# Kernel optimization log

Hardware: AMD Instinct MI355X
Metric: run time of the kernel (lower is better)

The kernel has to match this reference:

```python
import jax, jax.numpy as jnp
import numpy as np

B, G, T = 4096, 100, 24


def _greedy_dispatch(demand, caps, prices, slack_price):
    """Exact LP solution of: min prices@alloc + slack_price*slack
    s.t. 0<=alloc<=caps, sum(alloc)+slack = demand (per b,t).
    demand: [B,T] (nonneg), caps: [B,G,T], prices: [G], slack_price: scalar.
    Returns alloc [B,G,T], slack [B,T].
    """
    prices_all = jnp.concatenate([prices, slack_price[None]])        # [G+1]
    # slack capacity = demand itself (slack alone can absorb everything)
    caps_all = jnp.concatenate([caps, demand[:, None, :]], axis=1)    # [B,G+1,T]
    order = jnp.argsort(prices_all)                                   # merit order
    caps_s = caps_all[:, order, :]
    before = jnp.cumsum(caps_s, axis=1) - caps_s                      # capacity ahead in merit order
    alloc_s = jnp.clip(demand[:, None, :] - before, 0.0, caps_s)
    inv = jnp.argsort(order)
    alloc = alloc_s[:, inv, :]
    return alloc[:, :-1, :], alloc[:, -1, :]


def setup_inputs() -> dict:
    key = jax.random.key(0)
    k1, k2, k3, k4 = jax.random.split(key, 4)
    R_up = jax.random.uniform(k1, (B, G, T), dtype=jnp.float32)
    R_dn = jax.random.uniform(k2, (B, G, T), dtype=jnp.float32)
    omega_true = jax.random.normal(k3, (B, T), dtype=jnp.float32) * 5.0
    b_G = 10.0 + 40.0 * jax.random.uniform(k4, (G,), dtype=jnp.float32)  # marginal costs $/MWh
    return {
        "R_up": R_up,
        "R_dn": R_dn,
        "omega_true": omega_true,
        "b_G": b_G,
        "voll": jnp.float32(1000.0),
        "vosp": jnp.float32(500.0),
        "rt_up_ratio": jnp.float32(1.5),
        "rt_dn_ratio": jnp.float32(1.2),
    }


def reference(R_up, R_dn, omega_true, b_G, voll, vosp, rt_up_ratio, rt_dn_ratio):
    c_up = rt_up_ratio * b_G                                          # [G]
    c_dn = rt_dn_ratio * b_G                                          # [G]
    dem_up = jnp.maximum(omega_true, 0.0)                             # [B,T]
    dem_dn = jnp.maximum(-omega_true, 0.0)
    du, LS = _greedy_dispatch(dem_up, R_up, c_up, voll)
    dd, SP = _greedy_dispatch(dem_dn, R_dn, c_dn, vosp)
    rt_obj = (jnp.einsum('g,bgt->b', c_up, du)
              + jnp.einsum('g,bgt->b', c_dn, dd)
              + voll * LS.sum(axis=1) + vosp * SP.sum(axis=1))        # [B]
    return du, dd, LS, SP, rt_obj
```

## Files before the change

### kernel.cpp

```cpp
#include <hip/hip_runtime.h>

#define G_ 100
#define T_ 24
#define GP1 101
#define TILE (G_ * T_)
#define VPB (TILE / 4)
#define WPB 4
#define BLOCK (64 * WPB)

typedef float vfloat4 __attribute__((ext_vector_type(4)));

template<int N>
__device__ __forceinline__ void scan_chunk(int k0,
    const float* __restrict__ capp,
    int ord_lo, int ord_hi, float pr_lo, float pr_hi,
    float* __restrict__ ldscol,
    float dem, float& before, float& objp)
{
    int gg[N]; float pr[N], cap[N];
#pragma unroll
    for (int j = 0; j < N; ++j) {
        const int idx = k0 + j;
        if (idx < 64) {
            gg[j] = __builtin_amdgcn_readlane(ord_lo, idx);
            pr[j] = __int_as_float(__builtin_amdgcn_readlane(__float_as_int(pr_lo), idx));
        } else {
            gg[j] = __builtin_amdgcn_readlane(ord_hi, idx - 64);
            pr[j] = __int_as_float(__builtin_amdgcn_readlane(__float_as_int(pr_hi), idx - 64));
        }
    }
#pragma unroll
    for (int j = 0; j < N; ++j) cap[j] = capp[gg[j] * T_];
#pragma unroll
    for (int j = 0; j < N; ++j) {
        float a = fminf(fmaxf(dem - before, 0.f), cap[j]);
        before += cap[j];
        objp = fmaf(pr[j], a, objp);
        ldscol[gg[j] * T_] = a;
    }
}

__global__ __launch_bounds__(BLOCK, 4) void dispatch_kernel(
    const float* __restrict__ R_up, const float* __restrict__ R_dn,
    const float* __restrict__ omega,
    const float* __restrict__ b_G, const float* __restrict__ voll,
    const float* __restrict__ vosp, const float* __restrict__ ru,
    const float* __restrict__ rd,
    float* __restrict__ out, int B)
{
    __shared__ float s_tile[WPB * TILE];
    __shared__ float s_obj[WPB];

    const int tid  = threadIdx.x;

    if (tid < GP1) {
        float mu, md;
        if (tid < G_) { float bg = b_G[tid]; mu = ru[0] * bg; md = rd[0] * bg; }
        else          { mu = voll[0];        md = vosp[0]; }
        s_tile[tid] = mu; s_tile[128 + tid] = md;
    }
    __syncthreads();
    if (tid < GP1) {
        const float mu = s_tile[tid], md = s_tile[128 + tid];
        int r0 = 0, r1 = 0;
        for (int j = 0; j < GP1; ++j) {
            float vu = s_tile[j], vd = s_tile[128 + j];
            r0 += (vu < mu) || (vu == mu && j < tid);
            r1 += (vd < md) || (vd == md && j < tid);
        }
        ((int*)s_tile)[256 + r0] = tid;  s_tile[512 + r0] = mu;
        ((int*)s_tile)[384 + r1] = tid;  s_tile[640 + r1] = md;
    }
    __syncthreads();

    const int w    = tid >> 6;
    const int lane = tid & 63;
    const int b = __builtin_amdgcn_readfirstlane(blockIdx.x * 2 + (w >> 1));
    const int p = __builtin_amdgcn_readfirstlane(w & 1);
    const size_t bgt = (size_t)B * TILE;
    float* __restrict__ tw = &s_tile[w * TILE];

    const int hi_ok = (lane < GP1 - 64);
    const int   ord_lo = ((const int*)s_tile)[256 + p * 128 + lane];
    const int   ord_hi = hi_ok ? ((const int*)s_tile)[256 + p * 128 + 64 + lane] : 0;
    const float pr_lo  = s_tile[512 + p * 128 + lane];
    const float pr_hi  = hi_ok ? s_tile[512 + p * 128 + 64 + lane] : 0.f;
    __syncthreads();

#pragma unroll
    for (int j = 0; j < 9; ++j) *(vfloat4*)&tw[(lane + j * 64) * 4] = (vfloat4)(0.f);
    if (lane < VPB - 576)       *(vfloat4*)&tw[(lane + 576) * 4]    = (vfloat4)(0.f);

    const int t = (lane < T_) ? lane : 0;

    float objp = 0.f;
    if (lane < T_) {
        const float om  = omega[(size_t)b * T_ + t];
        const float dem = p ? fmaxf(-om, 0.f) : fmaxf(om, 0.f);
        const float* __restrict__ capp = (p ? R_dn : R_up) + (size_t)b * TILE + t;
        float* __restrict__ ldscol = tw + t;

        float before = 0.f;
        scan_chunk<16>( 0, capp, ord_lo, ord_hi, pr_lo, pr_hi, ldscol, dem, before, objp);
        bool run = __any(before < dem);
        if (run) { scan_chunk<16>(16, capp, ord_lo, ord_hi, pr_lo, pr_hi, ldscol, dem, before, objp);
                   run = __any(before < dem); }
        if (run) { scan_chunk< 8>(32, capp, ord_lo, ord_hi, pr_lo, pr_hi, ldscol, dem, before, objp);
                   run = __any(before < dem); }
        if (run) { scan_chunk< 8>(40, capp, ord_lo, ord_hi, pr_lo, pr_hi, ldscol, dem, before, objp);
                   run = __any(before < dem); }
        if (run) { scan_chunk< 8>(48, capp, ord_lo, ord_hi, pr_lo, pr_hi, ldscol, dem, before, objp);
                   run = __any(before < dem); }
        if (run) { scan_chunk< 8>(56, capp, ord_lo, ord_hi, pr_lo, pr_hi, ldscol, dem, before, objp);
                   run = __any(before < dem); }
        if (run) { scan_chunk< 8>(64, capp, ord_lo, ord_hi, pr_lo, pr_hi, ldscol, dem, before, objp);
                   run = __any(before < dem); }
        if (run) { scan_chunk< 8>(72, capp, ord_lo, ord_hi, pr_lo, pr_hi, ldscol, dem, before, objp);
                   run = __any(before < dem); }
        if (run) { scan_chunk< 8>(80, capp, ord_lo, ord_hi, pr_lo, pr_hi, ldscol, dem, before, objp);
                   run = __any(before < dem); }
        if (run) { scan_chunk< 8>(88, capp, ord_lo, ord_hi, pr_lo, pr_hi, ldscol, dem, before, objp);
                   run = __any(before < dem); }
        if (run)   scan_chunk< 4>(96, capp, ord_lo, ord_hi, pr_lo, pr_hi, ldscol, dem, before, objp);

        const float slack_pr =
            __int_as_float(__builtin_amdgcn_readlane(__float_as_int(pr_hi), GP1 - 1 - 64));
        float slackv = fmaxf(dem - before, 0.f);
        objp = fmaf(slack_pr, slackv, objp);
        out[2 * bgt + (size_t)p * B * T_ + (size_t)b * T_ + t] = slackv;
    }

#pragma unroll
    for (int off = 32; off; off >>= 1) objp += __shfl_xor(objp, off, 64);
    if (lane == 0) s_obj[w] = objp;

    __builtin_amdgcn_wave_barrier();
    {
        vfloat4* __restrict__ dst = (vfloat4*)out + ((size_t)p * B + b) * VPB;
#pragma unroll
        for (int j = 0; j < 9; ++j)
            dst[lane + j * 64] = *(const vfloat4*)&tw[(lane + j * 64) * 4];
        if (lane < VPB - 576)
            dst[lane + 576] = *(const vfloat4*)&tw[(lane + 576) * 4];
    }

    __syncthreads();
    if (tid == 0)
        out[2 * bgt + 2 * (size_t)B * T_ + b] = s_obj[0] + s_obj[1];
    if (tid == 128)
        out[2 * bgt + 2 * (size_t)B * T_ + b] = s_obj[2] + s_obj[3];
}

extern "C" void kernel_launch(void* const* d_in, const int* in_sizes, int n_in,
                              void* d_out, int out_size, void* d_ws, size_t ws_size,
                              hipStream_t stream)
{
    const float* R_up  = (const float*)d_in[0];
    const float* R_dn  = (const float*)d_in[1];
    const float* omega = (const float*)d_in[2];
    const float* b_G   = (const float*)d_in[3];
    const float* voll  = (const float*)d_in[4];
    const float* vosp  = (const float*)d_in[5];
    const float* ru    = (const float*)d_in[6];
    const float* rd    = (const float*)d_in[7];

    const int B = in_sizes[0] / TILE;
    float* out = (float*)d_out;

    dispatch_kernel<<<B / 2, BLOCK, 0, stream>>>(
        R_up, R_dn, omega, b_G, voll, vosp, ru, rd, out, B);
}
```

Baseline: 154.5 us.

## Write allocations directly to global memory, dropping LDS tile staging

Replaces the per-wave LDS tile (zero, scatter, then copy out) with a direct zero-fill of the output tile in global memory, followed by scattered global stores of the nonzero allocations. It also doubles batches per block to four, parallelizes the two merit-order rank computations across thread halves, and raises the launch bound occupancy hint. This frees a large amount of LDS so more blocks can be resident, but it adds uncoalesced scattered global writes and an explicit wait on the zero-fill so that ordering against the later stores is preserved.

Result: no change. 152.8 us (-1.1%).

```diff
diff --git a/kernel.cpp b/kernel.cpp
--- a/kernel.cpp
+++ b/kernel.cpp
@@ -5,7 +5,8 @@
 #define GP1 101
 #define TILE (G_ * T_)
 #define VPB (TILE / 4)
-#define WPB 4
+#define BPB 4
+#define WPB (BPB * 2)
 #define BLOCK (64 * WPB)
 
 typedef float vfloat4 __attribute__((ext_vector_type(4)));
@@ -13,8 +14,8 @@
 template<int N>
 __device__ __forceinline__ void scan_chunk(int k0,
     const float* __restrict__ capp,
+    float* __restrict__ gcol,
     int ord_lo, int ord_hi, float pr_lo, float pr_hi,
-    float* __restrict__ ldscol,
     float dem, float& before, float& objp)
 {
     int gg[N]; float pr[N], cap[N];
@@ -36,11 +37,11 @@
         float a = fminf(fmaxf(dem - before, 0.f), cap[j]);
         before += cap[j];
         objp = fmaf(pr[j], a, objp);
-        ldscol[gg[j] * T_] = a;
+        gcol[gg[j] * T_] = a;
     }
 }
 
-__global__ __launch_bounds__(BLOCK, 4) void dispatch_kernel(
+__global__ __launch_bounds__(BLOCK, 8) void dispatch_kernel(
     const float* __restrict__ R_up, const float* __restrict__ R_dn,
     const float* __restrict__ omega,
     const float* __restrict__ b_G, const float* __restrict__ voll,
@@ -48,48 +49,54 @@
     const float* __restrict__ rd,
     float* __restrict__ out, int B)
 {
-    __shared__ float s_tile[WPB * TILE];
-    __shared__ float s_obj[WPB];
+    __shared__ float s_praw[2][GP1];
+    __shared__ int   s_ord [2][128];
+    __shared__ float s_pr  [2][128];
+    __shared__ float s_obj [WPB];
 
-    const int tid  = threadIdx.x;
+    const int tid = threadIdx.x;
 
     if (tid < GP1) {
         float mu, md;
         if (tid < G_) { float bg = b_G[tid]; mu = ru[0] * bg; md = rd[0] * bg; }
         else          { mu = voll[0];        md = vosp[0]; }
-        s_tile[tid] = mu; s_tile[128 + tid] = md;
+        s_praw[0][tid] = mu; s_praw[1][tid] = md;
     }
     __syncthreads();
-    if (tid < GP1) {
-        const float mu = s_tile[tid], md = s_tile[128 + tid];
-        int r0 = 0, r1 = 0;
-        for (int j = 0; j < GP1; ++j) {
-            float vu = s_tile[j], vd = s_tile[128 + j];
-            r0 += (vu < mu) || (vu == mu && j < tid);
-            r1 += (vd < md) || (vd == md && j < tid);
+    {
+        const int pass = tid >> 8;
+        const int i    = tid & 255;
+        if (i < GP1) {
+            const float m = s_praw[pass][i];
+            int r = 0;
+            for (int j = 0; j < GP1; ++j) {
+                const float v = s_praw[pass][j];
+                r += (v < m) || (v == m && j < i);
+            }
+            s_ord[pass][r] = i;  s_pr[pass][r] = m;
         }
-        ((int*)s_tile)[256 + r0] = tid;  s_tile[512 + r0] = mu;
-        ((int*)s_tile)[384 + r1] = tid;  s_tile[640 + r1] = md;
     }
     __syncthreads();
 
     const int w    = tid >> 6;
     const int lane = tid & 63;
-    const int b = __builtin_amdgcn_readfirstlane(blockIdx.x * 2 + (w >> 1));
+    const int b = __builtin_amdgcn_readfirstlane(blockIdx.x * BPB + (w >> 1));
     const int p = __builtin_amdgcn_readfirstlane(w & 1);
     const size_t bgt = (size_t)B * TILE;
-    float* __restrict__ tw = &s_tile[w * TILE];
 
     const int hi_ok = (lane < GP1 - 64);
-    const int   ord_lo = ((const int*)s_tile)[256 + p * 128 + lane];
-    const int   ord_hi = hi_ok ? ((const int*)s_tile)[256 + p * 128 + 64 + lane] : 0;
-    const float pr_lo  = s_tile[512 + p * 128 + lane];
-    const float pr_hi  = hi_ok ? s_tile[512 + p * 128 + 64 + lane] : 0.f;
-    __syncthreads();
+    const int   ord_lo = s_ord[p][lane];
+    const int   ord_hi = hi_ok ? s_ord[p][64 + lane] : 0;
+    const float pr_lo  = s_pr [p][lane];
+    const float pr_hi  = hi_ok ? s_pr [p][64 + lane] : 0.f;
 
+    {
+        vfloat4* __restrict__ dst = (vfloat4*)out + ((size_t)p * B + b) * VPB;
 #pragma unroll
-    for (int j = 0; j < 9; ++j) *(vfloat4*)&tw[(lane + j * 64) * 4] = (vfloat4)(0.f);
-    if (lane < VPB - 576)       *(vfloat4*)&tw[(lane + 576) * 4]    = (vfloat4)(0.f);
+        for (int j = 0; j < 9; ++j) dst[lane + j * 64] = (vfloat4)(0.f);
+        if (lane < VPB - 576)       dst[lane + 576]    = (vfloat4)(0.f);
+    }
+    asm volatile("s_waitcnt vmcnt(0)" ::: "memory");
 
     const int t = (lane < T_) ? lane : 0;
 
@@ -98,30 +105,30 @@
         const float om  = omega[(size_t)b * T_ + t];
         const float dem = p ? fmaxf(-om, 0.f) : fmaxf(om, 0.f);
         const float* __restrict__ capp = (p ? R_dn : R_up) + (size_t)b * TILE + t;
-        float* __restrict__ ldscol = tw + t;
+        float* __restrict__ gcol = out + (size_t)p * bgt + (size_t)b * TILE + t;
 
         float before = 0.f;
-        scan_chunk<16>( 0, capp, ord_lo, ord_hi, pr_lo, pr_hi, ldscol, dem, before, objp);
+        scan_chunk<16>( 0, capp, gcol, ord_lo, ord_hi, pr_lo, pr_hi, dem, before, objp);
         bool run = __any(before < dem);
-        if (run) { scan_chunk<16>(16, capp, ord_lo, ord_hi, pr_lo, pr_hi, ldscol, dem, before, objp);
+        if (run) { scan_chunk<16>(16, capp, gcol, ord_lo, ord_hi, pr_lo, pr_hi, dem, before, objp);
                    run = __any(before < dem); }
-        if (run) { scan_chunk< 8>(32, capp, ord_lo, ord_hi, pr_lo, pr_hi, ldscol, dem, before, objp);
+        if (run) { scan_chunk< 8>(32, capp, gcol, ord_lo, ord_hi, pr_lo, pr_hi, dem, before, objp);
                    run = __any(before < dem); }
-        if (run) { scan_chunk< 8>(40, capp, ord_lo, ord_hi, pr_lo, pr_hi, ldscol, dem, before, objp);
+        if (run) { scan_chunk< 8>(40, capp, gcol, ord_lo, ord_hi, pr_lo, pr_hi, dem, before, objp);
                    run = __any(before < dem); }
-        if (run) { scan_chunk< 8>(48, capp, ord_lo, ord_hi, pr_lo, pr_hi, ldscol, dem, before, objp);
+        if (run) { scan_chunk< 8>(48, capp, gcol, ord_lo, ord_hi, pr_lo, pr_hi, dem, before, objp);
                    run = __any(before < dem); }
-        if (run) { scan_chunk< 8>(56, capp, ord_lo, ord_hi, pr_lo, pr_hi, ldscol, dem, before, objp);
+        if (run) { scan_chunk< 8>(56, capp, gcol, ord_lo, ord_hi, pr_lo, pr_hi, dem, before, objp);
                    run = __any(before < dem); }
-        if (run) { scan_chunk< 8>(64, capp, ord_lo, ord_hi, pr_lo, pr_hi, ldscol, dem, before, objp);
+        if (run) { scan_chunk< 8>(64, capp, gcol, ord_lo, ord_hi, pr_lo, pr_hi, dem, before, objp);
                    run = __any(before < dem); }
-        if (run) { scan_chunk< 8>(72, capp, ord_lo, ord_hi, pr_lo, pr_hi, ldscol, dem, before, objp);
+        if (run) { scan_chunk< 8>(72, capp, gcol, ord_lo, ord_hi, pr_lo, pr_hi, dem, before, objp);
                    run = __any(before < dem); }
-        if (run) { scan_chunk< 8>(80, capp, ord_lo, ord_hi, pr_lo, pr_hi, ldscol, dem, before, objp);
+        if (run) { scan_chunk< 8>(80, capp, gcol, ord_lo, ord_hi, pr_lo, pr_hi, dem, before, objp);
                    run = __any(before < dem); }
-        if (run) { scan_chunk< 8>(88, capp, ord_lo, ord_hi, pr_lo, pr_hi, ldscol, dem, before, objp);
+        if (run) { scan_chunk< 8>(88, capp, gcol, ord_lo, ord_hi, pr_lo, pr_hi, dem, before, objp);
                    run = __any(before < dem); }
-        if (run)   scan_chunk< 4>(96, capp, ord_lo, ord_hi, pr_lo, pr_hi, ldscol, dem, before, objp);
+        if (run)   scan_chunk< 4>(96, capp, gcol, ord_lo, ord_hi, pr_lo, pr_hi, dem, before, objp);
 
         const float slack_pr =
             __int_as_float(__builtin_amdgcn_readlane(__float_as_int(pr_hi), GP1 - 1 - 64));
@@ -134,21 +141,9 @@
     for (int off = 32; off; off >>= 1) objp += __shfl_xor(objp, off, 64);
     if (lane == 0) s_obj[w] = objp;
 
-    __builtin_amdgcn_wave_barrier();
-    {
-        vfloat4* __restrict__ dst = (vfloat4*)out + ((size_t)p * B + b) * VPB;
-#pragma unroll
-        for (int j = 0; j < 9; ++j)
-            dst[lane + j * 64] = *(const vfloat4*)&tw[(lane + j * 64) * 4];
-        if (lane < VPB - 576)
-            dst[lane + 576] = *(const vfloat4*)&tw[(lane + 576) * 4];
-    }
-
     __syncthreads();
-    if (tid == 0)
-        out[2 * bgt + 2 * (size_t)B * T_ + b] = s_obj[0] + s_obj[1];
-    if (tid == 128)
-        out[2 * bgt + 2 * (size_t)B * T_ + b] = s_obj[2] + s_obj[3];
+    if ((tid & 127) == 0)
+        out[2 * bgt + 2 * (size_t)B * T_ + b] = s_obj[w] + s_obj[w + 1];
 }
 
 extern "C" void kernel_launch(void* const* d_in, const int* in_sizes, int n_in,
@@ -167,6 +162,6 @@
     const int B = in_sizes[0] / TILE;
     float* out = (float*)d_out;
 
-    dispatch_kernel<<<B / 2, BLOCK, 0, stream>>>(
+    dispatch_kernel<<<B / BPB, BLOCK, 0, stream>>>(
         R_up, R_dn, omega, b_G, voll, vosp, ru, rd, out, B);
 }
```

## Stage capacity tile in LDS with coalesced loads and scan in place

Applied to the files above, without the earlier changes.

Each wave now loads its whole capacity tile from global memory with coalesced 16-byte loads into LDS. The merit-order scan then reads and overwrites capacities in LDS instead of issuing scattered global loads per generator. Because the scan runs all 100 generators unconditionally, the wave-wide early-exit checks and zero-fill are gone. The sort setup is also split so two groups of threads rank the up and down prices in parallel. The cost is that the full tile is always read and the serial scan has no early termination; LDS read-after-write within a wave relies on explicit waitcnt instead of a wave barrier.

Measured after the change: 164.2 us. +6.3%, slower.

```diff
diff --git a/kernel.cpp b/kernel.cpp
--- a/kernel.cpp
+++ b/kernel.cpp
@@ -10,36 +10,6 @@
 
 typedef float vfloat4 __attribute__((ext_vector_type(4)));
 
-template<int N>
-__device__ __forceinline__ void scan_chunk(int k0,
-    const float* __restrict__ capp,
-    int ord_lo, int ord_hi, float pr_lo, float pr_hi,
-    float* __restrict__ ldscol,
-    float dem, float& before, float& objp)
-{
-    int gg[N]; float pr[N], cap[N];
-#pragma unroll
-    for (int j = 0; j < N; ++j) {
-        const int idx = k0 + j;
-        if (idx < 64) {
-            gg[j] = __builtin_amdgcn_readlane(ord_lo, idx);
-            pr[j] = __int_as_float(__builtin_amdgcn_readlane(__float_as_int(pr_lo), idx));
-        } else {
-            gg[j] = __builtin_amdgcn_readlane(ord_hi, idx - 64);
-            pr[j] = __int_as_float(__builtin_amdgcn_readlane(__float_as_int(pr_hi), idx - 64));
-        }
-    }
-#pragma unroll
-    for (int j = 0; j < N; ++j) cap[j] = capp[gg[j] * T_];
-#pragma unroll
-    for (int j = 0; j < N; ++j) {
-        float a = fminf(fmaxf(dem - before, 0.f), cap[j]);
-        before += cap[j];
-        objp = fmaf(pr[j], a, objp);
-        ldscol[gg[j] * T_] = a;
-    }
-}
-
 __global__ __launch_bounds__(BLOCK, 4) void dispatch_kernel(
     const float* __restrict__ R_up, const float* __restrict__ R_dn,
     const float* __restrict__ omega,
@@ -51,25 +21,30 @@
     __shared__ float s_tile[WPB * TILE];
     __shared__ float s_obj[WPB];
 
-    const int tid  = threadIdx.x;
+    const int tid = threadIdx.x;
 
-    if (tid < GP1) {
-        float mu, md;
-        if (tid < G_) { float bg = b_G[tid]; mu = ru[0] * bg; md = rd[0] * bg; }
-        else          { mu = voll[0];        md = vosp[0]; }
-        s_tile[tid] = mu; s_tile[128 + tid] = md;
+    float* s_praw = s_tile;
+    int*   s_ord  = (int*)&s_tile[256];
+    float* s_pr   = &s_tile[512];
+
+    const int sp = tid >> 7;
+    const int si = tid & 127;
+    if (si < GP1) {
+        float m;
+        if (si < G_) m = (sp ? rd[0] : ru[0]) * b_G[si];
+        else         m = sp ? vosp[0] : voll[0];
+        s_praw[sp * GP1 + si] = m;
     }
     __syncthreads();
-    if (tid < GP1) {
-        const float mu = s_tile[tid], md = s_tile[128 + tid];
-        int r0 = 0, r1 = 0;
+    if (si < GP1) {
+        const float m = s_praw[sp * GP1 + si];
+        int r = 0;
         for (int j = 0; j < GP1; ++j) {
-            float vu = s_tile[j], vd = s_tile[128 + j];
-            r0 += (vu < mu) || (vu == mu && j < tid);
-            r1 += (vd < md) || (vd == md && j < tid);
+            const float v = s_praw[sp * GP1 + j];
+            r += (v < m) || (v == m && j < si);
         }
-        ((int*)s_tile)[256 + r0] = tid;  s_tile[512 + r0] = mu;
-        ((int*)s_tile)[384 + r1] = tid;  s_tile[640 + r1] = md;
+        s_ord[sp * 128 + r] = si;
+        s_pr [sp * 128 + r] = m;
     }
     __syncthreads();
 
@@ -78,54 +53,50 @@
     const int b = __builtin_amdgcn_readfirstlane(blockIdx.x * 2 + (w >> 1));
     const int p = __builtin_amdgcn_readfirstlane(w & 1);
     const size_t bgt = (size_t)B * TILE;
-    float* __restrict__ tw = &s_tile[w * TILE];
 
     const int hi_ok = (lane < GP1 - 64);
-    const int   ord_lo = ((const int*)s_tile)[256 + p * 128 + lane];
-    const int   ord_hi = hi_ok ? ((const int*)s_tile)[256 + p * 128 + 64 + lane] : 0;
-    const float pr_lo  = s_tile[512 + p * 128 + lane];
-    const float pr_hi  = hi_ok ? s_tile[512 + p * 128 + 64 + lane] : 0.f;
+    const int   ord_lo = s_ord[p * 128 + lane];
+    const int   ord_hi = hi_ok ? s_ord[p * 128 + 64 + lane] : 0;
+    const float pr_lo  = s_pr [p * 128 + lane];
+    const float pr_hi  = hi_ok ? s_pr [p * 128 + 64 + lane] : 0.f;
     __syncthreads();
 
+    float* __restrict__ tw = &s_tile[w * TILE];
+    {
+        const vfloat4* __restrict__ s4 =
+            (const vfloat4*)((p ? R_dn : R_up) + (size_t)b * TILE);
+        vfloat4 v[9]; vfloat4 vt;
 #pragma unroll
-    for (int j = 0; j < 9; ++j) *(vfloat4*)&tw[(lane + j * 64) * 4] = (vfloat4)(0.f);
-    if (lane < VPB - 576)       *(vfloat4*)&tw[(lane + 576) * 4]    = (vfloat4)(0.f);
-
-    const int t = (lane < T_) ? lane : 0;
+        for (int j = 0; j < 9; ++j) v[j] = s4[lane + j * 64];
+        if (lane < VPB - 576) vt = s4[lane + 576];
+#pragma unroll
+        for (int j = 0; j < 9; ++j) *(vfloat4*)&tw[(lane + j * 64) * 4] = v[j];
+        if (lane < VPB - 576) *(vfloat4*)&tw[(lane + 576) * 4] = vt;
+    }
+    asm volatile("s_waitcnt lgkmcnt(0)" ::: "memory");
 
     float objp = 0.f;
     if (lane < T_) {
+        const int t = lane;
         const float om  = omega[(size_t)b * T_ + t];
         const float dem = p ? fmaxf(-om, 0.f) : fmaxf(om, 0.f);
-        const float* __restrict__ capp = (p ? R_dn : R_up) + (size_t)b * TILE + t;
-        float* __restrict__ ldscol = tw + t;
-
         float before = 0.f;
-        scan_chunk<16>( 0, capp, ord_lo, ord_hi, pr_lo, pr_hi, ldscol, dem, before, objp);
-        bool run = __any(before < dem);
-        if (run) { scan_chunk<16>(16, capp, ord_lo, ord_hi, pr_lo, pr_hi, ldscol, dem, before, objp);
-                   run = __any(before < dem); }
-        if (run) { scan_chunk< 8>(32, capp, ord_lo, ord_hi, pr_lo, pr_hi, ldscol, dem, before, objp);
-                   run = __any(before < dem); }
-        if (run) { scan_chunk< 8>(40, capp, ord_lo, ord_hi, pr_lo, pr_hi, ldscol, dem, before, objp);
-                   run = __any(before < dem); }
-        if (run) { scan_chunk< 8>(48, capp, ord_lo, ord_hi, pr_lo, pr_hi, ldscol, dem, before, objp);
-                   run = __any(before < dem); }
-        if (run) { scan_chunk< 8>(56, capp, ord_lo, ord_hi, pr_lo, pr_hi, ldscol, dem, before, objp);
-                   run = __any(before < dem); }
-        if (run) { scan_chunk< 8>(64, capp, ord_lo, ord_hi, pr_lo, pr_hi, ldscol, dem, before, objp);
-                   run = __any(before < dem); }
-        if (run) { scan_chunk< 8>(72, capp, ord_lo, ord_hi, pr_lo, pr_hi, ldscol, dem, before, objp);
-                   run = __any(before < dem); }
-        if (run) { scan_chunk< 8>(80, capp, ord_lo, ord_hi, pr_lo, pr_hi, ldscol, dem, before, objp);
-                   run = __any(before < dem); }
-        if (run) { scan_chunk< 8>(88, capp, ord_lo, ord_hi, pr_lo, pr_hi, ldscol, dem, before, objp);
-                   run = __any(before < dem); }
-        if (run)   scan_chunk< 4>(96, capp, ord_lo, ord_hi, pr_lo, pr_hi, ldscol, dem, before, objp);
-
+#pragma unroll
+        for (int r = 0; r < G_; ++r) {
+            const int g = (r < 64) ? __builtin_amdgcn_readlane(ord_lo, r)
+                                   : __builtin_amdgcn_readlane(ord_hi, r - 64);
+            const float prr = (r < 64)
+                ? __int_as_float(__builtin_amdgcn_readlane(__float_as_int(pr_lo), r))
+                : __int_as_float(__builtin_amdgcn_readlane(__float_as_int(pr_hi), r - 64));
+            const float cap = tw[g * T_ + t];
+            const float a = fminf(fmaxf(dem - before, 0.f), cap);
+            before += cap;
+            objp = fmaf(prr, a, objp);
+            tw[g * T_ + t] = a;
+        }
         const float slack_pr =
             __int_as_float(__builtin_amdgcn_readlane(__float_as_int(pr_hi), GP1 - 1 - 64));
-        float slackv = fmaxf(dem - before, 0.f);
+        const float slackv = fmaxf(dem - before, 0.f);
         objp = fmaf(slack_pr, slackv, objp);
         out[2 * bgt + (size_t)p * B * T_ + (size_t)b * T_ + t] = slackv;
     }
@@ -134,7 +105,7 @@
     for (int off = 32; off; off >>= 1) objp += __shfl_xor(objp, off, 64);
     if (lane == 0) s_obj[w] = objp;
 
-    __builtin_amdgcn_wave_barrier();
+    asm volatile("s_waitcnt lgkmcnt(0)" ::: "memory");
     {
         vfloat4* __restrict__ dst = (vfloat4*)out + ((size_t)p * B + b) * VPB;
 #pragma unroll
```
